# Kernel optimization log

Hardware: AMD Instinct MI355X
Metric: run time of the kernel (lower is better)

The kernel has to match this reference:

```python
import jax, jax.numpy as jnp
import numpy as np
import math

B, C, BINS, W = 2, 8, 1024, 512
HEADS = 16
HD = BINS // HEADS          # 64 head dim
ROT = BINS // HEADS // 2    # 32 rotated dims
EXP = 4
EPS = 1e-5
MAX_FREQ = 10.0


def setup_inputs() -> dict:
    key = jax.random.key(0)
    ks = jax.random.split(key, 8)
    def u(k, shape, fan_in):
        lim = 1.0 / math.sqrt(fan_in)
        return jax.random.uniform(k, shape, jnp.float32, -lim, lim)
    return {
        "x": jax.random.normal(ks[0], (B, C, BINS, W), jnp.float32),
        "norm1_w": jnp.ones((BINS,), jnp.float32),
        "norm1_b": jnp.zeros((BINS,), jnp.float32),
        # 'pixel' rotary init: linspace(1, max_freq/2, dim//2) * pi (learned)
        "rot_freqs": jnp.linspace(1.0, MAX_FREQ / 2, ROT // 2, dtype=jnp.float32) * math.pi,
        "q_w": u(ks[1], (C, BINS, BINS), BINS),
        "out_w": u(ks[2], (C, BINS, BINS), BINS),
        "norm2_w": jnp.ones((BINS,), jnp.float32),
        "norm2_b": jnp.zeros((BINS,), jnp.float32),
        "lin1_w": u(ks[3], (C, BINS * EXP, BINS), BINS),
        "lin2_w": u(ks[4], (C, BINS, BINS * EXP), BINS * EXP),
    }


def _mlin(x, w):
    # x: [b,c,f_in,w]; w: [c,f_out,f_in] -> [b,c,f_out,w]
    return jnp.einsum('bcfw,cgf->bcgw', x, w)


def _frame_norm(x, w, b):
    # LayerNorm over the bins axis (axis=2) of [b,c,bins,w]
    m = jnp.mean(x, axis=2, keepdims=True)
    v = jnp.var(x, axis=2, keepdims=True)
    xn = (x - m) * jax.lax.rsqrt(v + EPS)
    return xn * w[:, None] + b[:, None]


def _rotate(q, cos, sin):
    # q: [b,c,h,w,d]; rotate first ROT dims with interleaved-pair rotate_half
    q1, q2 = q[..., :ROT], q[..., ROT:]
    qp = q1.reshape(*q1.shape[:-1], ROT // 2, 2)
    rh = jnp.stack([-qp[..., 1], qp[..., 0]], axis=-1).reshape(q1.shape)
    return jnp.concatenate([q1 * cos + rh * sin, q2], axis=-1)


def _attention(x, rot_freqs, q_w, out_w):
    b, c, bins, w = x.shape
    # faithful to source: q, k, v ALL use q_proj
    y = _mlin(x, q_w)  # [b,c,bins,w]
    # -> [b,c,h,w,d]
    y = y.transpose(0, 1, 3, 2).reshape(b, c, w, HEADS, HD).transpose(0, 1, 3, 2, 4)
    # rotary angles: t * freqs, repeat-interleaved x2 -> [w, ROT]
    t = jnp.arange(w, dtype=jnp.float32)
    ang = jnp.repeat(t[:, None] * rot_freqs[None, :], 2, axis=-1)
    cos, sin = jnp.cos(ang), jnp.sin(ang)
    q = _rotate(y, cos, sin)
    k = _rotate(y, cos, sin)
    v = y
    # NOTE: source scales by 1/sqrt(h) where h == bins (spectral height)
    scores = jnp.einsum('bchwd,bchud->bchwu', q, k) / math.sqrt(bins)
    a = jnp.einsum('bchwu,bchud->bchwd', jax.nn.softmax(scores, axis=-1), v)
    # [b,c,h,w,d] -> [b,c,bins,w]
    a = a.transpose(0, 1, 3, 2, 4).reshape(b, c, w, bins).transpose(0, 1, 3, 2)
    return _mlin(a, out_w)


def reference(x, norm1_w, norm1_b, rot_freqs, q_w, out_w,
              norm2_w, norm2_b, lin1_w, lin2_w):
    z = _frame_norm(x, norm1_w, norm1_b)
    z = _attention(z, rot_freqs, q_w, out_w)
    x = x + z  # dropout=0 -> identity
    z = _frame_norm(x, norm2_w, norm2_b)
    z = _mlin(jax.nn.gelu(_mlin(z, lin1_w), approximate=False), lin2_w)
    return x + z
```

## Files before the change

### kernel.cpp

```cpp
#include <hip/hip_runtime.h>
#include <math.h>

#define BB 2
#define CCH 8
#define BINS 1024
#define WW 512
#define HEADS 16
#define HD 64
#define ROTD 32
#define EXPF 4
#define NXE 8388608L
#define NTW 32

typedef unsigned short ushortT;
typedef short bf16x8 __attribute__((ext_vector_type(8)));
typedef float f32x4 __attribute__((ext_vector_type(4)));

__device__ __forceinline__ ushortT f2bf(float f) {
    unsigned int u = __float_as_uint(f);
    u = (u + 0x7FFF + ((u >> 16) & 1)) >> 16;
    return (ushortT)u;
}
__device__ __forceinline__ float bf2f(ushortT h) {
    return __uint_as_float(((unsigned int)h) << 16);
}
__device__ __forceinline__ unsigned int cvtpk(float lo, float hi) {
    unsigned int r;
    asm("v_cvt_pk_bf16_f32 %0, %1, %2" : "=v"(r) : "v"(lo), "v"(hi));
    return r;
}
__device__ __forceinline__ float geluf(float x) {
    return 0.5f * x * (1.f + erff(x * 0.70710678118654752f));
}
__device__ __forceinline__ void gl_lds16(const ushortT* g, ushortT* l) {
    __builtin_amdgcn_global_load_lds(
        (const __attribute__((address_space(1))) unsigned int*)g,
        (__attribute__((address_space(3))) unsigned int*)l, 16, 0, 0);
}

__global__ __launch_bounds__(256)
void wcast_k(const float* __restrict__ s, ushortT* __restrict__ d, long n)
{
    long i = ((long)blockIdx.x * 256 + threadIdx.x) * 8;
    if (i >= n) return;
    float4 a = *(const float4*)&s[i];
    float4 b = *(const float4*)&s[i + 4];
    uint4 v;
    v.x = cvtpk(a.x, a.y); v.y = cvtpk(a.z, a.w);
    v.z = cvtpk(b.x, b.y); v.w = cvtpk(b.z, b.w);
    *(uint4*)&d[i] = v;
}

__global__ __launch_bounds__(1024)
void normT_k(const float* __restrict__ X, const float* __restrict__ wgt,
             const float* __restrict__ bia, ushortT* __restrict__ YT)
{
    __shared__ float tile[NTW][BINS + 1];
    __shared__ float red0[32][NTW], red1[32][NTW];
    __shared__ float ms[NTW], is[NTW];
    const int bc = blockIdx.x >> 4;
    const int w0 = (blockIdx.x & 15) * NTW;
    const int tid = threadIdx.x;
    const int w  = tid & (NTW - 1);
    const int fy = tid >> 5;
    const float* Xb = X + (long)bc * BINS * WW + w0;
    float s = 0.f, s2 = 0.f;
    for (int f = fy; f < BINS; f += 32) {
        float v = Xb[(long)f * WW + w];
        s += v; s2 += v * v;
        tile[w][f] = v;
    }
    red0[fy][w] = s; red1[fy][w] = s2;
    __syncthreads();
    if (tid < NTW) {
        float ss = 0.f, qq = 0.f;
        #pragma unroll
        for (int j = 0; j < 32; ++j) { ss += red0[j][tid]; qq += red1[j][tid]; }
        float m = ss * (1.f / BINS);
        float var = qq * (1.f / BINS) - m * m;
        ms[tid] = m; is[tid] = rsqrtf(var + 1e-5f);
    }
    __syncthreads();
    const int w2 = tid >> 5;
    const int c  = tid & 31;
    float m = ms[w2], inv = is[w2];
    ushortT* Yb = YT + ((long)bc * WW + w0 + w2) * BINS;
    #pragma unroll
    for (int jj = 0; jj < 4; ++jj) {
        int f0 = jj * 256 + c * 8;
        union { ushortT h[8]; uint4 v; } r;
        #pragma unroll
        for (int e = 0; e < 8; ++e) {
            int f = f0 + e;
            float v = (tile[w2][f] - m) * inv * wgt[f] + bia[f];
            r.h[e] = f2bf(v);
        }
        *(uint4*)&Yb[f0] = r.v;
    }
}

__global__ void rope_tab_k(const float* __restrict__ freqs,
                           float* __restrict__ cosT, float* __restrict__ sinT)
{
    int idx = blockIdx.x * 256 + threadIdx.x;
    if (idx >= WW * 16) return;
    int w = idx >> 4, i = idx & 15;
    float ang = (float)w * freqs[i];
    cosT[idx] = cosf(ang);
    sinT[idx] = sinf(ang);
}

__global__ __launch_bounds__(256)
void mattn_k(const ushortT* __restrict__ rotT, const ushortT* __restrict__ yT,
             ushortT* __restrict__ oT)
{
    __shared__ ushortT Qs[64 * 64];
    __shared__ ushortT Ks[64 * 64];
    __shared__ ushortT Vs[64 * 72];
    __shared__ ushortT Ps[64 * 72];
    const int z = blockIdx.y;
    const int bc = z >> 4, h = z & 15;
    const int wq0 = blockIdx.x * 64;
    const int tid = threadIdx.x;
    const int wv = tid >> 6, l = tid & 63;
    const int lr = l & 15, lk = l >> 4;
    const long hbase = (long)bc * WW * 1024 + h * 64;

    #pragma unroll
    for (int p = 0; p < 2; ++p) {
        int r0 = p * 32 + wv * 8;
        int row = r0 + (l >> 3);
        int gs = (l & 7) ^ (row & 7);
        gl_lds16(rotT + hbase + (long)(wq0 + row) * 1024 + gs * 8, Qs + r0 * 64);
    }

    f32x4 oacc[4] = {};
    float mrow[4] = {-INFINITY, -INFINITY, -INFINITY, -INFINITY};
    float lrow[4] = {0.f, 0.f, 0.f, 0.f};

    for (int u0 = 0; u0 < WW; u0 += 64) {
        #pragma unroll
        for (int p = 0; p < 2; ++p) {
            int r0 = p * 32 + wv * 8;
            int row = r0 + (l >> 3);
            int gs = (l & 7) ^ (row & 7);
            gl_lds16(rotT + hbase + (long)(u0 + row) * 1024 + gs * 8, Ks + r0 * 64);
        }
        #pragma unroll
        for (int rep = 0; rep < 2; ++rep) {
            int ch = rep * 4 + wv;
            union { uint4 v; ushortT h8[8]; } tmp;
            tmp.v = *(const uint4*)(yT + hbase + (long)(u0 + l) * 1024 + ch * 8);
            #pragma unroll
            for (int j = 0; j < 8; ++j)
                Vs[(ch * 8 + j) * 72 + l] = tmp.h8[j];
        }
        __syncthreads();

        f32x4 sacc[4] = {};
        #pragma unroll
        for (int ko = 0; ko < 2; ++ko) {
            int ar = wv * 16 + lr;
            bf16x8 aq = *(const bf16x8*)&Qs[ar * 64 + (((ko * 4) + lk) ^ (ar & 7)) * 8];
            #pragma unroll
            for (int f = 0; f < 4; ++f) {
                int br = f * 16 + lr;
                bf16x8 bk = *(const bf16x8*)&Ks[br * 64 + (((ko * 4) + lk) ^ (br & 7)) * 8];
                sacc[f] = __builtin_amdgcn_mfma_f32_16x16x32_bf16(aq, bk, sacc[f], 0, 0, 0);
            }
        }

        #pragma unroll
        for (int rg = 0; rg < 4; ++rg) {
            float s0 = sacc[0][rg] * (1.f / 32.f);
            float s1 = sacc[1][rg] * (1.f / 32.f);
            float s2 = sacc[2][rg] * (1.f / 32.f);
            float s3 = sacc[3][rg] * (1.f / 32.f);
            float mx = fmaxf(fmaxf(s0, s1), fmaxf(s2, s3));
            mx = fmaxf(mx, __shfl_xor(mx, 1));
            mx = fmaxf(mx, __shfl_xor(mx, 2));
            mx = fmaxf(mx, __shfl_xor(mx, 4));
            mx = fmaxf(mx, __shfl_xor(mx, 8));
            float mnew = fmaxf(mrow[rg], mx);
            float al = __expf(mrow[rg] - mnew);
            float p0 = __expf(s0 - mnew), p1 = __expf(s1 - mnew);
            float p2 = __expf(s2 - mnew), p3 = __expf(s3 - mnew);
            float rs = p0 + p1 + p2 + p3;
            rs += __shfl_xor(rs, 1);
            rs += __shfl_xor(rs, 2);
            rs += __shfl_xor(rs, 4);
            rs += __shfl_xor(rs, 8);
            lrow[rg] = lrow[rg] * al + rs;
            mrow[rg] = mnew;
            oacc[0][rg] *= al; oacc[1][rg] *= al;
            oacc[2][rg] *= al; oacc[3][rg] *= al;
            int prow = wv * 16 + lk * 4 + rg;
            Ps[prow * 72 +  0 + lr] = f2bf(p0);
            Ps[prow * 72 + 16 + lr] = f2bf(p1);
            Ps[prow * 72 + 32 + lr] = f2bf(p2);
            Ps[prow * 72 + 48 + lr] = f2bf(p3);
        }
        asm volatile("s_waitcnt lgkmcnt(0)" ::: "memory");

        #pragma unroll
        for (int ko = 0; ko < 2; ++ko) {
            int ar = wv * 16 + lr;
            bf16x8 ap = *(const bf16x8*)&Ps[ar * 72 + ko * 32 + lk * 8];
            #pragma unroll
            for (int f = 0; f < 4; ++f) {
                bf16x8 bv = *(const bf16x8*)&Vs[(f * 16 + lr) * 72 + ko * 32 + lk * 8];
                oacc[f] = __builtin_amdgcn_mfma_f32_16x16x32_bf16(ap, bv, oacc[f], 0, 0, 0);
            }
        }
        __syncthreads();
    }

    #pragma unroll
    for (int rg = 0; rg < 4; ++rg) {
        float inv = 1.f / lrow[rg];
        int w = wq0 + wv * 16 + lk * 4 + rg;
        long b2 = (long)bc * WW * 1024 + (long)w * 1024 + h * 64;
        #pragma unroll
        for (int f = 0; f < 4; ++f)
            oT[b2 + f * 16 + lr] = f2bf(oacc[f][rg] * inv);
    }
}

#define QPHASE(QM, QN, STAGES, VMW)                                          \
  {                                                                          \
    bf16x8 a0_[4], a1_[4], b0_[2], b1_[2];                                   \
    _Pragma("unroll")                                                        \
    for (int i = 0; i < 4; ++i) {                                            \
        int ra = wr * 128 + QM * 64 + i * 16 + lrow;                         \
        a0_[i] = *(const bf16x8*)&As[ra * 64 + ((lk    ) ^ (ra & 7)) * 8];   \
        a1_[i] = *(const bf16x8*)&As[ra * 64 + ((lk + 4) ^ (ra & 7)) * 8];   \
    }                                                                        \
    _Pragma("unroll")                                                        \
    for (int j = 0; j < 2; ++j) {                                            \
        int rb = wc * 64 + QN * 32 + j * 16 + lrow;                          \
        b0_[j] = *(const bf16x8*)&Bs[rb * 64 + ((lk    ) ^ (rb & 7)) * 8];   \
        b1_[j] = *(const bf16x8*)&Bs[rb * 64 + ((lk + 4) ^ (rb & 7)) * 8];   \
    }                                                                        \
    STAGES;                                                                  \
    VMW;                                                                     \
    asm volatile("s_waitcnt lgkmcnt(0)" ::: "memory");                       \
    __builtin_amdgcn_s_barrier();                                            \
    __builtin_amdgcn_s_setprio(1);                                           \
    _Pragma("unroll")                                                        \
    for (int i = 0; i < 4; ++i)                                              \
        _Pragma("unroll")                                                    \
        for (int j = 0; j < 2; ++j)                                          \
            acc[QM * 4 + i][QN * 2 + j] =                                    \
                __builtin_amdgcn_mfma_f32_16x16x32_bf16(                     \
                    a0_[i], b0_[j], acc[QM * 4 + i][QN * 2 + j], 0, 0, 0);   \
    _Pragma("unroll")                                                        \
    for (int i = 0; i < 4; ++i)                                              \
        _Pragma("unroll")                                                    \
        for (int j = 0; j < 2; ++j)                                          \
            acc[QM * 4 + i][QN * 2 + j] =                                    \
                __builtin_amdgcn_mfma_f32_16x16x32_bf16(                     \
                    a1_[i], b1_[j], acc[QM * 4 + i][QN * 2 + j], 0, 0, 0);   \
    __builtin_amdgcn_s_setprio(0);                                           \
  }

template<bool HASRES, bool GELUF, bool TRANSOUT>
__global__ __launch_bounds__(512)
void gemm8_k(const ushortT* __restrict__ A, long sA, int aMod,
             const ushortT* __restrict__ B, long sB,
             void* __restrict__ Cp, long sC,
             const float* __restrict__ R, long sR,
             int M, int N, int K, int gx, int gy)
{
    __shared__ ushortT smem[65536];
    const int nwg = gridDim.x;
    const int bid = blockIdx.x;
    const int lid = (bid & 7) * (nwg >> 3) + (bid >> 3);
    const int x = lid % gx;
    const int y = (lid / gx) % gy;
    const int z = lid / (gx * gy);
    const ushortT* Ab = A + (long)(z % aMod) * sA + (long)y * 256 * K;
    const ushortT* Bb = B + (long)z * sB + (long)x * 256 * K;
    const int tid = threadIdx.x;
    const int wv = tid >> 6, l = tid & 63;
    const int lrow = l & 15, lk = l >> 4;
    const int wr = wv >> 2, wc = wv & 3;
    f32x4 acc[8][4] = {};
    const int NT = K >> 6;

    auto stageAh = [&](int T, int qm) {
        ushortT* D = smem + (T & 1) * 32768;
        const int k0 = T << 6;
        #pragma unroll
        for (int t = 0; t < 2; ++t) {
            int r0 = wv * 16 + t * 8;
            int gr0 = ((r0 & 64) << 1) + qm * 64 + (r0 & 63);
            int gr = gr0 + (l >> 3);
            int gs = (l & 7) ^ (gr & 7);
            gl_lds16(Ab + (long)gr * K + k0 + gs * 8, D + gr0 * 64);
        }
    };
    auto stageBh = [&](int T, int qn) {
        ushortT* D = smem + (T & 1) * 32768 + 16384;
        const int k0 = T << 6;
        #pragma unroll
        for (int t = 0; t < 2; ++t) {
            int r0 = wv * 16 + t * 8;
            int gr0 = ((r0 >> 5) << 6) + qn * 32 + (r0 & 31);
            int gr = gr0 + (l >> 3);
            int gs = (l & 7) ^ (gr & 7);
            gl_lds16(Bb + (long)gr * K + k0 + gs * 8, D + gr0 * 64);
        }
    };

    stageAh(0, 0); stageAh(0, 1); stageBh(0, 0); stageBh(0, 1);
    if (NT > 1) {
        stageAh(1, 0); stageBh(1, 0);
        asm volatile("s_waitcnt vmcnt(4)" ::: "memory");
    } else {
        asm volatile("s_waitcnt vmcnt(0)" ::: "memory");
    }
    __builtin_amdgcn_s_barrier();

    for (int T = 0; T < NT; ++T) {
        const ushortT* As = smem + (T & 1) * 32768;
        const ushortT* Bs = As + 16384;
        const bool s1 = (T + 1 < NT), s2 = (T + 2 < NT);
        QPHASE(0, 0, if (s1) stageAh(T + 1, 1), );
        QPHASE(0, 1, if (s1) stageBh(T + 1, 1), );
        QPHASE(1, 0, if (s2) stageAh(T + 2, 0), );
        QPHASE(1, 1, if (s2) stageBh(T + 2, 0),
               if (s2) { asm volatile("s_waitcnt vmcnt(4)" ::: "memory"); }
               else    { asm volatile("s_waitcnt vmcnt(0)" ::: "memory"); });
    }

    const int m0g = y * 256 + wr * 128, n0g = x * 256 + wc * 64;
    if (!TRANSOUT) {
        float* Cf = (float*)Cp + (long)z * sC;
        #pragma unroll
        for (int ip = 0; ip < 8; ++ip)
            #pragma unroll
            for (int j = 0; j < 4; ++j)
                #pragma unroll
                for (int rg = 0; rg < 4; ++rg) {
                    long m = m0g + ip * 16 + lk * 4 + rg;
                    long n = n0g + j * 16 + lrow;
                    float v = acc[ip][j][rg];
                    if (GELUF) v = geluf(v);
                    if (HASRES) v += R[(long)z * sR + m * N + n];
                    Cf[m * N + n] = v;
                }
    } else {
        __syncthreads();
        ushortT* Ts = smem + wv * 4096;
        ushortT* CT = (ushortT*)Cp + (long)z * sC;
        #pragma unroll
        for (int s = 0; s < 2; ++s) {
            #pragma unroll
            for (int i2 = 0; i2 < 4; ++i2)
                #pragma unroll
                for (int j = 0; j < 4; ++j)
                    #pragma unroll
                    for (int rg = 0; rg < 4; ++rg) {
                        int ml = i2 * 16 + lk * 4 + rg;
                        int nl = j * 16 + lrow;
                        float v = acc[s * 4 + i2][j][rg];
                        if (GELUF) v = geluf(v);
                        Ts[nl * 64 + (((ml >> 3) ^ (nl & 7)) << 3) + (ml & 7)] = f2bf(v);
                    }
            #pragma unroll
            for (int p = 0; p < 8; ++p) {
                int nl = p * 8 + (l >> 3), mc = l & 7;
                uint4 d = *(const uint4*)&Ts[nl * 64 + ((mc ^ (nl & 7)) << 3)];
                *(uint4*)&CT[(long)(n0g + nl) * M + m0g + s * 64 + mc * 8] = d;
            }
        }
    }
}

template<bool HASRES, bool GELUF, bool TRANSOUT>
__global__ __launch_bounds__(512)
void pgemm_k(const ushortT* __restrict__ A, long sA, int aMod,
             const ushortT* __restrict__ B, long sB,
             void* __restrict__ Cp, long sC,
             const float* __restrict__ R, long sR,
             int M, int N, int K, int gx, int gy)
{
    __shared__ ushortT smem[3 * 24576];
    const int nwg = gridDim.x;
    const int bid = blockIdx.x;
    const int lid = (bid & 7) * (nwg >> 3) + (bid >> 3);
    const int x = lid % gx;
    const int y = (lid / gx) % gy;
    const int z = lid / (gx * gy);
    const ushortT* Ab = A + (long)(z % aMod) * sA + (long)y * 128 * K;
    const ushortT* Bb = B + (long)z * sB + (long)x * 256 * K;
    const int tid = threadIdx.x;
    const int wv = tid >> 6, l = tid & 63;
    const int lrow = l & 15, lk = l >> 4;
    const int mb = (wv >> 2) * 64;
    const int nb = (wv & 3) * 64;
    f32x4 acc[4][4] = {};
    const int NT = K >> 6;

    auto stage = [&](int T) {
        ushortT* S = smem + (T % 3) * 24576;
        ushortT* As = S;
        ushortT* Bs = S + 8192;
        const int k0 = T << 6;
        #pragma unroll
        for (int t = 0; t < 2; ++t) {
            int r0 = wv * 16 + t * 8;
            int row = r0 + (l >> 3);
            int gs = (l & 7) ^ (row & 7);
            gl_lds16(Ab + (long)row * K + k0 + gs * 8, As + r0 * 64);
        }
        #pragma unroll
        for (int t = 0; t < 4; ++t) {
            int r0 = wv * 32 + t * 8;
            int row = r0 + (l >> 3);
            int gs = (l & 7) ^ (row & 7);
            gl_lds16(Bb + (long)row * K + k0 + gs * 8, Bs + r0 * 64);
        }
    };
    auto compute = [&](int T) {
        const ushortT* S = smem + (T % 3) * 24576;
        const ushortT* As = S;
        const ushortT* Bs = S + 8192;
        #pragma unroll
        for (int ko = 0; ko < 2; ++ko) {
            bf16x8 af[4], bg[4];
            #pragma unroll
            for (int i = 0; i < 4; ++i) {
                int ra = mb + i * 16 + lrow;
                af[i] = *(const bf16x8*)&As[ra * 64 + ((lk + ko * 4) ^ (ra & 7)) * 8];
                int rb = nb + i * 16 + lrow;
                bg[i] = *(const bf16x8*)&Bs[rb * 64 + ((lk + ko * 4) ^ (rb & 7)) * 8];
            }
            #pragma unroll
            for (int i = 0; i < 4; ++i)
                #pragma unroll
                for (int j = 0; j < 4; ++j)
                    acc[i][j] = __builtin_amdgcn_mfma_f32_16x16x32_bf16(
                        af[i], bg[j], acc[i][j], 0, 0, 0);
        }
    };

    stage(0);
    if (NT > 1) {
        stage(1);
        asm volatile("s_waitcnt vmcnt(6)" ::: "memory");
    } else {
        asm volatile("s_waitcnt vmcnt(0)" ::: "memory");
    }
    __builtin_amdgcn_s_barrier();

    for (int T = 0; T < NT; ++T) {
        if (T + 2 < NT) stage(T + 2);
        compute(T);
        if (T + 1 < NT) {
            if (T + 2 < NT) asm volatile("s_waitcnt vmcnt(6)" ::: "memory");
            else            asm volatile("s_waitcnt vmcnt(0)" ::: "memory");
            __builtin_amdgcn_s_barrier();
        }
    }

    const int m0g = y * 128 + mb, n0g = x * 256 + nb;
    if (!TRANSOUT) {
        float* Cf = (float*)Cp + (long)z * sC;
        #pragma unroll
        for (int i = 0; i < 4; ++i)
            #pragma unroll
            for (int j = 0; j < 4; ++j)
                #pragma unroll
                for (int rg = 0; rg < 4; ++rg) {
                    long m = m0g + i * 16 + lk * 4 + rg;
                    long n = n0g + j * 16 + lrow;
                    float v = acc[i][j][rg];
                    if (GELUF) v = geluf(v);
                    if (HASRES) v += R[(long)z * sR + m * N + n];
                    Cf[m * N + n] = v;
                }
    } else {
        __syncthreads();
        ushortT* Ts = smem + wv * 4096;
        #pragma unroll
        for (int i = 0; i < 4; ++i)
            #pragma unroll
            for (int j = 0; j < 4; ++j)
                #pragma unroll
                for (int rg = 0; rg < 4; ++rg) {
                    int ml = i * 16 + lk * 4 + rg;
                    int nl = j * 16 + lrow;
                    float v = acc[i][j][rg];
                    if (GELUF) v = geluf(v);
                    Ts[nl * 64 + (((ml >> 3) ^ (nl & 7)) << 3) + (ml & 7)] = f2bf(v);
                }
        __syncthreads();
        ushortT* CT = (ushortT*)Cp + (long)z * sC;
        #pragma unroll
        for (int p = 0; p < 8; ++p) {
            int nl = p * 8 + (l >> 3), mc = l & 7;
            uint4 d = *(const uint4*)&Ts[nl * 64 + ((mc ^ (nl & 7)) << 3)];
            *(uint4*)&CT[(long)(n0g + nl) * M + m0g + mc * 8] = d;
        }
    }
}

template<bool HASRES, bool GELUF, bool TRANSOUT, bool ROPE>
__global__ __launch_bounds__(256)
void fgemm_k(const float* __restrict__ A, long sA, int aMod,
             const ushortT* __restrict__ B, long sB,
             void* __restrict__ Cp, long sC,
             const float* __restrict__ R, long sR,
             ushortT* __restrict__ Crot,
             const float* __restrict__ cosT, const float* __restrict__ sinT,
             int M, int N, int K, int gx, int gy)
{
    __shared__ ushortT smem[2 * 8192];
    ushortT* As = smem;
    ushortT* Bs = smem + 8192;
    const int nwg = gridDim.x;
    const int bid = blockIdx.x;
    const int lid = (bid & 7) * (nwg >> 3) + (bid >> 3);
    const int x = lid % gx;
    const int y = (lid / gx) % gy;
    const int z = lid / (gx * gy);
    const float*   Ab = A + (long)(z % aMod) * sA + (long)y * 128 * K;
    const ushortT* Bb = B + (long)z * sB + (long)x * 128 * K;
    const int tid = threadIdx.x;
    const int wv = tid >> 6, l = tid & 63;
    const int lrow = l & 15, lk = l >> 4;
    const int mb = (wv >> 1) * 64, nb = (wv & 1) * 64;
    const int arow = tid >> 3, agrp = tid & 7;
    f32x4 acc[4][4] = {};
    float4 a0[4], a1[4];
    const int NT = K >> 6;

    auto fetchA = [&](int k0) {
        #pragma unroll
        for (int c = 0; c < 4; ++c) {
            const float* src = Ab + (long)(arow + c * 32) * K + k0 + agrp * 8;
            a0[c] = *(const float4*)src;
            a1[c] = *(const float4*)(src + 4);
        }
    };
    auto commitA = [&]() {
        #pragma unroll
        for (int c = 0; c < 4; ++c) {
            int row = arow + c * 32;
            uint4 v;
            v.x = cvtpk(a0[c].x, a0[c].y);
            v.y = cvtpk(a0[c].z, a0[c].w);
            v.z = cvtpk(a1[c].x, a1[c].y);
            v.w = cvtpk(a1[c].z, a1[c].w);
            *(uint4*)&As[row * 64 + ((agrp ^ (row & 7)) << 3)] = v;
        }
    };
    auto stageB = [&](int k0) {
        #pragma unroll
        for (int t = 0; t < 4; ++t) {
            int r0 = wv * 32 + t * 8;
            int row = r0 + (l >> 3);
            int gs = (l & 7) ^ (row & 7);
            gl_lds16(Bb + (long)row * K + k0 + gs * 8, Bs + r0 * 64);
        }
    };
    auto compute = [&]() {
        #pragma unroll
        for (int ko = 0; ko < 2; ++ko) {
            bf16x8 af[4], bg[4];
            #pragma unroll
            for (int i = 0; i < 4; ++i) {
                int ra = mb + i * 16 + lrow;
                af[i] = *(const bf16x8*)&As[ra * 64 + ((lk + ko * 4) ^ (ra & 7)) * 8];
                int rb = nb + i * 16 + lrow;
                bg[i] = *(const bf16x8*)&Bs[rb * 64 + ((lk + ko * 4) ^ (rb & 7)) * 8];
            }
            #pragma unroll
            for (int i = 0; i < 4; ++i)
                #pragma unroll
                for (int j = 0; j < 4; ++j)
                    acc[i][j] = __builtin_amdgcn_mfma_f32_16x16x32_bf16(
                        af[i], bg[j], acc[i][j], 0, 0, 0);
        }
    };

    fetchA(0);
    for (int t = 0; t < NT; ++t) {
        if (t > 0) __syncthreads();
        stageB(t << 6);
        commitA();
        if (t + 1 < NT) fetchA((t + 1) << 6);
        __syncthreads();
        compute();
    }

    const int m0g = y * 128 + mb, n0g = x * 128 + nb;
    if (!TRANSOUT) {
        float* Cf = (float*)Cp + (long)z * sC;
        #pragma unroll
        for (int i = 0; i < 4; ++i)
            #pragma unroll
            for (int j = 0; j < 4; ++j)
                #pragma unroll
                for (int rg = 0; rg < 4; ++rg) {
                    long m = m0g + i * 16 + lk * 4 + rg;
                    long n = n0g + j * 16 + lrow;
                    float v = acc[i][j][rg];
                    if (GELUF) v = geluf(v);
                    if (HASRES) v += R[(long)z * sR + m * N + n];
                    Cf[m * N + n] = v;
                }
    } else {
        ushortT* Ts = smem + wv * 4096;
        __syncthreads();
        #pragma unroll
        for (int i = 0; i < 4; ++i)
            #pragma unroll
            for (int j = 0; j < 4; ++j)
                #pragma unroll
                for (int rg = 0; rg < 4; ++rg) {
                    int ml = i * 16 + lk * 4 + rg;
                    int nl = j * 16 + lrow;
                    float v = acc[i][j][rg];
                    if (GELUF) v = geluf(v);
                    Ts[nl * 64 + (((ml >> 3) ^ (nl & 7)) << 3) + (ml & 7)] = f2bf(v);
                }
        __syncthreads();
        ushortT* CT = (ushortT*)Cp + (long)z * sC;
        #pragma unroll
        for (int p = 0; p < 8; ++p) {
            int nl = p * 8 + (l >> 3), mc = l & 7;
            uint4 d = *(const uint4*)&Ts[nl * 64 + ((mc ^ (nl & 7)) << 3)];
            int wg = n0g + nl;
            int g0 = m0g + mc * 8;
            *(uint4*)&CT[(long)wg * M + g0] = d;
            if (ROPE) {
                ushortT* RT = Crot + (long)z * sC;
                int d0 = g0 & 63;
                if (d0 >= ROTD) {
                    *(uint4*)&RT[(long)wg * M + g0] = d;
                } else {
                    union { uint4 v; ushortT h8[8]; } in, ov;
                    in.v = d;
                    #pragma unroll
                    for (int j = 0; j < 8; j += 2) {
                        int i2 = (d0 + j) >> 1;
                        float cc = cosT[wg * 16 + i2], ss = sinT[wg * 16 + i2];
                        float a = bf2f(in.h8[j]), b = bf2f(in.h8[j + 1]);
                        ov.h8[j]     = f2bf(a * cc - b * ss);
                        ov.h8[j + 1] = f2bf(b * cc + a * ss);
                    }
                    *(uint4*)&RT[(long)wg * M + g0] = ov.v;
                }
            }
        }
    }
}

extern "C" void kernel_launch(void* const* d_in, const int* in_sizes, int n_in,
                              void* d_out, int out_size, void* d_ws, size_t ws_size,
                              hipStream_t stream)
{
    const float* x    = (const float*)d_in[0];
    const float* n1w  = (const float*)d_in[1];
    const float* n1b  = (const float*)d_in[2];
    const float* freqs= (const float*)d_in[3];
    const float* qw   = (const float*)d_in[4];
    const float* ow   = (const float*)d_in[5];
    const float* n2w  = (const float*)d_in[6];
    const float* n2b  = (const float*)d_in[7];
    const float* l1w  = (const float*)d_in[8];
    const float* l2w  = (const float*)d_in[9];
    float* out = (float*)d_out;
    char* wsb  = (char*)d_ws;
    const long MB = 1L << 20;

    ushortT* znT  = (ushortT*)(wsb +   0 * MB);
    ushortT* yT   = (ushortT*)(wsb +  16 * MB);
    ushortT* rotT = (ushortT*)(wsb +  32 * MB);
    ushortT* CfT  = (ushortT*)(wsb +  48 * MB);
    ushortT* wB   = (ushortT*)(wsb +   0 * MB);
    ushortT* zn2T = (ushortT*)(wsb +  64 * MB);
    ushortT* h1T  = (ushortT*)(wsb +  80 * MB);
    float*   cosT = (float*)  (wsb + 144 * MB);
    float*   sinT = cosT + WW * 16;

    rope_tab_k<<<32, 256, 0, stream>>>(freqs, cosT, sinT);

    normT_k<<<BB * CCH * 16, 1024, 0, stream>>>(x, n1w, n1b, znT);

    fgemm_k<false, false, true, true><<<512, 256, 0, stream>>>(
        qw,  (long)BINS * BINS, CCH,
        znT, (long)WW * BINS,
        yT,  (long)WW * BINS,
        nullptr, 0,
        rotT, cosT, sinT,
        BINS, WW, BINS, 4, 8);

    mattn_k<<<dim3(8, 256), 256, 0, stream>>>(rotT, yT, CfT);

    fgemm_k<true, false, false, false><<<512, 256, 0, stream>>>(
        ow,  (long)BINS * BINS, CCH,
        CfT, (long)WW * BINS,
        out, (long)BINS * WW,
        x,   (long)BINS * WW,
        nullptr, nullptr, nullptr,
        BINS, WW, BINS, 4, 8);

    wcast_k<<<16384, 256, 0, stream>>>(l1w, wB, 8L * BINS * EXPF * BINS);

    normT_k<<<BB * CCH * 16, 1024, 0, stream>>>(out, n2w, n2b, zn2T);

    gemm8_k<false, true, true><<<512, 512, 0, stream>>>(
        wB,   (long)BINS * EXPF * BINS, CCH,
        zn2T, (long)WW * BINS,
        h1T,  (long)WW * BINS * EXPF,
        nullptr, 0,
        BINS * EXPF, WW, BINS, 2, 16);

    wcast_k<<<16384, 256, 0, stream>>>(l2w, wB, 8L * BINS * EXPF * BINS);

    pgemm_k<true, false, false><<<256, 512, 0, stream>>>(
        wB,  (long)BINS * BINS * EXPF, CCH,
        h1T, (long)WW * BINS * EXPF,
        out, (long)BINS * WW,
        out, (long)BINS * WW,
        BINS, WW, BINS * EXPF, 2, 8);
}
```

Before: 428.6 us.

## Fuse fp32-to-bf16 weight casting into MLP GEMM A-tile staging

Removes the two standalone weight-cast kernels for lin1 and lin2 weights. The GEMMs now load fp32 weights into registers, convert them to bf16, and write swizzled tiles to LDS. The register prefetch is interleaved with the existing multi-stage pipeline. This avoids writing and re-reading 64MB of bf16 weights. In exchange, each A tile reads twice the bytes per GEMM, uses extra registers, and issues synchronous LDS stores in place of direct global-to-LDS loads, with adjusted waitcnt values.

```diff
diff --git a/kernel.cpp b/kernel.cpp
--- a/kernel.cpp
+++ b/kernel.cpp
@@ -36,19 +36,6 @@
     __builtin_amdgcn_global_load_lds(
         (const __attribute__((address_space(1))) unsigned int*)g,
         (__attribute__((address_space(3))) unsigned int*)l, 16, 0, 0);
-}
-
-__global__ __launch_bounds__(256)
-void wcast_k(const float* __restrict__ s, ushortT* __restrict__ d, long n)
-{
-    long i = ((long)blockIdx.x * 256 + threadIdx.x) * 8;
-    if (i >= n) return;
-    float4 a = *(const float4*)&s[i];
-    float4 b = *(const float4*)&s[i + 4];
-    uint4 v;
-    v.x = cvtpk(a.x, a.y); v.y = cvtpk(a.z, a.w);
-    v.z = cvtpk(b.x, b.y); v.w = cvtpk(b.z, b.w);
-    *(uint4*)&d[i] = v;
 }
 
 __global__ __launch_bounds__(1024)
@@ -265,11 +252,11 @@
 
 template<bool HASRES, bool GELUF, bool TRANSOUT>
 __global__ __launch_bounds__(512)
-void gemm8_k(const ushortT* __restrict__ A, long sA, int aMod,
-             const ushortT* __restrict__ B, long sB,
-             void* __restrict__ Cp, long sC,
-             const float* __restrict__ R, long sR,
-             int M, int N, int K, int gx, int gy)
+void gemm8f_k(const float* __restrict__ A, long sA, int aMod,
+              const ushortT* __restrict__ B, long sB,
+              void* __restrict__ Cp, long sC,
+              const float* __restrict__ R, long sR,
+              int M, int N, int K, int gx, int gy)
 {
     __shared__ ushortT smem[65536];
     const int nwg = gridDim.x;
@@ -278,25 +265,39 @@
     const int x = lid % gx;
     const int y = (lid / gx) % gy;
     const int z = lid / (gx * gy);
-    const ushortT* Ab = A + (long)(z % aMod) * sA + (long)y * 256 * K;
+    const float*   Ab = A + (long)(z % aMod) * sA + (long)y * 256 * K;
     const ushortT* Bb = B + (long)z * sB + (long)x * 256 * K;
     const int tid = threadIdx.x;
     const int wv = tid >> 6, l = tid & 63;
     const int lrow = l & 15, lk = l >> 4;
     const int wr = wv >> 2, wc = wv & 3;
     f32x4 acc[8][4] = {};
+    float4 rA[8];
     const int NT = K >> 6;
 
-    auto stageAh = [&](int T, int qm) {
+    auto fetchA = [&](int T) {
+        const int k0 = T << 6;
+        #pragma unroll
+        for (int c = 0; c < 4; ++c) {
+            int idx = tid + c * 512;
+            int row = idx >> 3, grp = idx & 7;
+            const float* src = Ab + (long)row * K + k0 + grp * 8;
+            rA[c * 2]     = *(const float4*)src;
+            rA[c * 2 + 1] = *(const float4*)(src + 4);
+        }
+    };
+    auto commitA = [&](int T) {
         ushortT* D = smem + (T & 1) * 32768;
-        const int k0 = T << 6;
-        #pragma unroll
-        for (int t = 0; t < 2; ++t) {
-            int r0 = wv * 16 + t * 8;
-            int gr0 = ((r0 & 64) << 1) + qm * 64 + (r0 & 63);
-            int gr = gr0 + (l >> 3);
-            int gs = (l & 7) ^ (gr & 7);
-            gl_lds16(Ab + (long)gr * K + k0 + gs * 8, D + gr0 * 64);
+        #pragma unroll
+        for (int c = 0; c < 4; ++c) {
+            int idx = tid + c * 512;
+            int row = idx >> 3, grp = idx & 7;
+            uint4 v;
+            v.x = cvtpk(rA[c * 2].x,     rA[c * 2].y);
+            v.y = cvtpk(rA[c * 2].z,     rA[c * 2].w);
+            v.z = cvtpk(rA[c * 2 + 1].x, rA[c * 2 + 1].y);
+            v.w = cvtpk(rA[c * 2 + 1].z, rA[c * 2 + 1].w);
+            *(uint4*)&D[row * 64 + ((grp ^ (row & 7)) << 3)] = v;
         }
     };
     auto stageBh = [&](int T, int qn) {
@@ -312,12 +313,15 @@
         }
     };
 
-    stageAh(0, 0); stageAh(0, 1); stageBh(0, 0); stageBh(0, 1);
+    fetchA(0);
+    commitA(0);
+    stageBh(0, 0); stageBh(0, 1);
     if (NT > 1) {
-        stageAh(1, 0); stageBh(1, 0);
-        asm volatile("s_waitcnt vmcnt(4)" ::: "memory");
+        fetchA(1);
+        stageBh(1, 0);
+        asm volatile("s_waitcnt vmcnt(10) lgkmcnt(0)" ::: "memory");
     } else {
-        asm volatile("s_waitcnt vmcnt(0)" ::: "memory");
+        asm volatile("s_waitcnt vmcnt(0) lgkmcnt(0)" ::: "memory");
     }
     __builtin_amdgcn_s_barrier();
 
@@ -325,11 +329,11 @@
         const ushortT* As = smem + (T & 1) * 32768;
         const ushortT* Bs = As + 16384;
         const bool s1 = (T + 1 < NT), s2 = (T + 2 < NT);
-        QPHASE(0, 0, if (s1) stageAh(T + 1, 1), );
+        QPHASE(0, 0, if (s1) commitA(T + 1), );
         QPHASE(0, 1, if (s1) stageBh(T + 1, 1), );
-        QPHASE(1, 0, if (s2) stageAh(T + 2, 0), );
+        QPHASE(1, 0, if (s2) fetchA(T + 2), );
         QPHASE(1, 1, if (s2) stageBh(T + 2, 0),
-               if (s2) { asm volatile("s_waitcnt vmcnt(4)" ::: "memory"); }
+               if (s2) { asm volatile("s_waitcnt vmcnt(10)" ::: "memory"); }
                else    { asm volatile("s_waitcnt vmcnt(0)" ::: "memory"); });
     }
 
@@ -379,11 +383,11 @@
 
 template<bool HASRES, bool GELUF, bool TRANSOUT>
 __global__ __launch_bounds__(512)
-void pgemm_k(const ushortT* __restrict__ A, long sA, int aMod,
-             const ushortT* __restrict__ B, long sB,
-             void* __restrict__ Cp, long sC,
-             const float* __restrict__ R, long sR,
-             int M, int N, int K, int gx, int gy)
+void pgemmf_k(const float* __restrict__ A, long sA, int aMod,
+              const ushortT* __restrict__ B, long sB,
+              void* __restrict__ Cp, long sC,
+              const float* __restrict__ R, long sR,
+              int M, int N, int K, int gx, int gy)
 {
     __shared__ ushortT smem[3 * 24576];
     const int nwg = gridDim.x;
@@ -392,7 +396,7 @@
     const int x = lid % gx;
     const int y = (lid / gx) % gy;
     const int z = lid / (gx * gy);
-    const ushortT* Ab = A + (long)(z % aMod) * sA + (long)y * 128 * K;
+    const float*   Ab = A + (long)(z % aMod) * sA + (long)y * 128 * K;
     const ushortT* Bb = B + (long)z * sB + (long)x * 256 * K;
     const int tid = threadIdx.x;
     const int wv = tid >> 6, l = tid & 63;
@@ -400,20 +404,37 @@
     const int mb = (wv >> 2) * 64;
     const int nb = (wv & 3) * 64;
     f32x4 acc[4][4] = {};
+    float4 rA[4];
     const int NT = K >> 6;
 
-    auto stage = [&](int T) {
-        ushortT* S = smem + (T % 3) * 24576;
-        ushortT* As = S;
-        ushortT* Bs = S + 8192;
+    auto fetchA = [&](int T) {
         const int k0 = T << 6;
         #pragma unroll
-        for (int t = 0; t < 2; ++t) {
-            int r0 = wv * 16 + t * 8;
-            int row = r0 + (l >> 3);
-            int gs = (l & 7) ^ (row & 7);
-            gl_lds16(Ab + (long)row * K + k0 + gs * 8, As + r0 * 64);
-        }
+        for (int c = 0; c < 2; ++c) {
+            int idx = tid + c * 512;
+            int row = idx >> 3, grp = idx & 7;
+            const float* src = Ab + (long)row * K + k0 + grp * 8;
+            rA[c * 2]     = *(const float4*)src;
+            rA[c * 2 + 1] = *(const float4*)(src + 4);
+        }
+    };
+    auto commitA = [&](int T) {
+        ushortT* As = smem + (T % 3) * 24576;
+        #pragma unroll
+        for (int c = 0; c < 2; ++c) {
+            int idx = tid + c * 512;
+            int row = idx >> 3, grp = idx & 7;
+            uint4 v;
+            v.x = cvtpk(rA[c * 2].x,     rA[c * 2].y);
+            v.y = cvtpk(rA[c * 2].z,     rA[c * 2].w);
+            v.z = cvtpk(rA[c * 2 + 1].x, rA[c * 2 + 1].y);
+            v.w = cvtpk(rA[c * 2 + 1].z, rA[c * 2 + 1].w);
+            *(uint4*)&As[row * 64 + ((grp ^ (row & 7)) << 3)] = v;
+        }
+    };
+    auto stageB = [&](int T) {
+        ushortT* Bs = smem + (T % 3) * 24576 + 8192;
+        const int k0 = T << 6;
         #pragma unroll
         for (int t = 0; t < 4; ++t) {
             int r0 = wv * 32 + t * 8;
@@ -445,21 +466,23 @@
         }
     };
 
-    stage(0);
+    fetchA(0); commitA(0); stageB(0);
     if (NT > 1) {
-        stage(1);
-        asm volatile("s_waitcnt vmcnt(6)" ::: "memory");
+        fetchA(1); stageB(1);
+        asm volatile("s_waitcnt vmcnt(8) lgkmcnt(0)" ::: "memory");
     } else {
-        asm volatile("s_waitcnt vmcnt(0)" ::: "memory");
+        asm volatile("s_waitcnt vmcnt(0) lgkmcnt(0)" ::: "memory");
     }
     __builtin_amdgcn_s_barrier();
 
     for (int T = 0; T < NT; ++T) {
-        if (T + 2 < NT) stage(T + 2);
+        const bool s1 = (T + 1 < NT), s2 = (T + 2 < NT);
+        if (s1) commitA(T + 1);
+        if (s2) { fetchA(T + 2); stageB(T + 2); }
         compute(T);
-        if (T + 1 < NT) {
-            if (T + 2 < NT) asm volatile("s_waitcnt vmcnt(6)" ::: "memory");
-            else            asm volatile("s_waitcnt vmcnt(0)" ::: "memory");
+        if (s1) {
+            if (s2) asm volatile("s_waitcnt vmcnt(8) lgkmcnt(0)" ::: "memory");
+            else    asm volatile("s_waitcnt vmcnt(0) lgkmcnt(0)" ::: "memory");
             __builtin_amdgcn_s_barrier();
         }
     }
@@ -680,7 +703,6 @@
     ushortT* yT   = (ushortT*)(wsb +  16 * MB);
     ushortT* rotT = (ushortT*)(wsb +  32 * MB);
     ushortT* CfT  = (ushortT*)(wsb +  48 * MB);
-    ushortT* wB   = (ushortT*)(wsb +   0 * MB);
     ushortT* zn2T = (ushortT*)(wsb +  64 * MB);
     ushortT* h1T  = (ushortT*)(wsb +  80 * MB);
     float*   cosT = (float*)  (wsb + 144 * MB);
@@ -708,21 +730,17 @@
         nullptr, nullptr, nullptr,
         BINS, WW, BINS, 4, 8);
 
-    wcast_k<<<16384, 256, 0, stream>>>(l1w, wB, 8L * BINS * EXPF * BINS);
-
     normT_k<<<BB * CCH * 16, 1024, 0, stream>>>(out, n2w, n2b, zn2T);
 
-    gemm8_k<false, true, true><<<512, 512, 0, stream>>>(
-        wB,   (long)BINS * EXPF * BINS, CCH,
+    gemm8f_k<false, true, true><<<512, 512, 0, stream>>>(
+        l1w,  (long)BINS * EXPF * BINS, CCH,
         zn2T, (long)WW * BINS,
         h1T,  (long)WW * BINS * EXPF,
         nullptr, 0,
         BINS * EXPF, WW, BINS, 2, 16);
 
-    wcast_k<<<16384, 256, 0, stream>>>(l2w, wB, 8L * BINS * EXPF * BINS);
-
-    pgemm_k<true, false, false><<<256, 512, 0, stream>>>(
-        wB,  (long)BINS * BINS * EXPF, CCH,
+    pgemmf_k<true, false, false><<<256, 512, 0, stream>>>(
+        l2w, (long)BINS * BINS * EXPF, CCH,
         h1T, (long)WW * BINS * EXPF,
         out, (long)BINS * WW,
         out, (long)BINS * WW,
```

After: 466.9 us. 8.9% more time.

## Interleave global-to-LDS staging with MFMA phases and raise MFMA priority

Applied to the files above, without the earlier changes.

Restructures the GEMM main loop into two half-K phases. Each phase loads its fragments from LDS, then issues part of the next-next tile's global-to-LDS copies, barriers, and runs the MFMAs under s_setprio(1). The aim is to spread memory issue across compute and keep waves in lockstep so MFMA and loads overlap better. In exchange it adds a barrier per half-tile, which costs extra synchronisation.

```diff
diff --git a/kernel.cpp b/kernel.cpp
--- a/kernel.cpp
+++ b/kernel.cpp
@@ -402,10 +402,8 @@
     f32x4 acc[4][4] = {};
     const int NT = K >> 6;
 
-    auto stage = [&](int T) {
-        ushortT* S = smem + (T % 3) * 24576;
-        ushortT* As = S;
-        ushortT* Bs = S + 8192;
+    auto stageA = [&](int T) {
+        ushortT* As = smem + (T % 3) * 24576;
         const int k0 = T << 6;
         #pragma unroll
         for (int t = 0; t < 2; ++t) {
@@ -414,53 +412,78 @@
             int gs = (l & 7) ^ (row & 7);
             gl_lds16(Ab + (long)row * K + k0 + gs * 8, As + r0 * 64);
         }
-        #pragma unroll
-        for (int t = 0; t < 4; ++t) {
-            int r0 = wv * 32 + t * 8;
+    };
+    auto stageBh = [&](int T, int h) {
+        ushortT* Bs = smem + (T % 3) * 24576 + 8192;
+        const int k0 = T << 6;
+        #pragma unroll
+        for (int t = 0; t < 2; ++t) {
+            int r0 = wv * 32 + (h * 2 + t) * 8;
             int row = r0 + (l >> 3);
             int gs = (l & 7) ^ (row & 7);
             gl_lds16(Bb + (long)row * K + k0 + gs * 8, Bs + r0 * 64);
         }
     };
-    auto compute = [&](int T) {
-        const ushortT* S = smem + (T % 3) * 24576;
-        const ushortT* As = S;
-        const ushortT* Bs = S + 8192;
-        #pragma unroll
-        for (int ko = 0; ko < 2; ++ko) {
+
+    stageA(0); stageBh(0, 0); stageBh(0, 1);
+    if (NT > 1) {
+        stageA(1); stageBh(1, 0); stageBh(1, 1);
+        asm volatile("s_waitcnt vmcnt(6)" ::: "memory");
+    } else {
+        asm volatile("s_waitcnt vmcnt(0)" ::: "memory");
+    }
+    __builtin_amdgcn_s_barrier();
+
+    for (int T = 0; T < NT; ++T) {
+        const ushortT* As = smem + (T % 3) * 24576;
+        const ushortT* Bs = As + 8192;
+        const bool s1 = (T + 1 < NT), s2 = (T + 2 < NT);
+
+        {
             bf16x8 af[4], bg[4];
             #pragma unroll
             for (int i = 0; i < 4; ++i) {
                 int ra = mb + i * 16 + lrow;
-                af[i] = *(const bf16x8*)&As[ra * 64 + ((lk + ko * 4) ^ (ra & 7)) * 8];
+                af[i] = *(const bf16x8*)&As[ra * 64 + ((lk) ^ (ra & 7)) * 8];
                 int rb = nb + i * 16 + lrow;
-                bg[i] = *(const bf16x8*)&Bs[rb * 64 + ((lk + ko * 4) ^ (rb & 7)) * 8];
+                bg[i] = *(const bf16x8*)&Bs[rb * 64 + ((lk) ^ (rb & 7)) * 8];
             }
+            if (s2) { stageA(T + 2); stageBh(T + 2, 0); }
+            asm volatile("s_waitcnt lgkmcnt(0)" ::: "memory");
+            __builtin_amdgcn_s_barrier();
+            __builtin_amdgcn_s_setprio(1);
             #pragma unroll
             for (int i = 0; i < 4; ++i)
                 #pragma unroll
                 for (int j = 0; j < 4; ++j)
                     acc[i][j] = __builtin_amdgcn_mfma_f32_16x16x32_bf16(
                         af[i], bg[j], acc[i][j], 0, 0, 0);
-        }
-    };
-
-    stage(0);
-    if (NT > 1) {
-        stage(1);
-        asm volatile("s_waitcnt vmcnt(6)" ::: "memory");
-    } else {
-        asm volatile("s_waitcnt vmcnt(0)" ::: "memory");
-    }
-    __builtin_amdgcn_s_barrier();
-
-    for (int T = 0; T < NT; ++T) {
-        if (T + 2 < NT) stage(T + 2);
-        compute(T);
-        if (T + 1 < NT) {
-            if (T + 2 < NT) asm volatile("s_waitcnt vmcnt(6)" ::: "memory");
-            else            asm volatile("s_waitcnt vmcnt(0)" ::: "memory");
+            __builtin_amdgcn_s_setprio(0);
+        }
+        {
+            bf16x8 af[4], bg[4];
+            #pragma unroll
+            for (int i = 0; i < 4; ++i) {
+                int ra = mb + i * 16 + lrow;
+                af[i] = *(const bf16x8*)&As[ra * 64 + ((lk + 4) ^ (ra & 7)) * 8];
+                int rb = nb + i * 16 + lrow;
+                bg[i] = *(const bf16x8*)&Bs[rb * 64 + ((lk + 4) ^ (rb & 7)) * 8];
+            }
+            if (s2) stageBh(T + 2, 1);
+            if (s1) {
+                if (s2) { asm volatile("s_waitcnt vmcnt(6)" ::: "memory"); }
+                else    { asm volatile("s_waitcnt vmcnt(0)" ::: "memory"); }
+            }
+            asm volatile("s_waitcnt lgkmcnt(0)" ::: "memory");
             __builtin_amdgcn_s_barrier();
+            __builtin_amdgcn_s_setprio(1);
+            #pragma unroll
+            for (int i = 0; i < 4; ++i)
+                #pragma unroll
+                for (int j = 0; j < 4; ++j)
+                    acc[i][j] = __builtin_amdgcn_mfma_f32_16x16x32_bf16(
+                        af[i], bg[j], acc[i][j], 0, 0, 0);
+            __builtin_amdgcn_s_setprio(0);
         }
     }
 
```

Result: no change. 428.8 us (+0.0%).
